# Kernel tuning notes

Measured on AMD Instinct MI355X. Metric: run time of the kernel, lower is better.

The kernel has to match this reference:

```python
import jax, jax.numpy as jnp
import numpy as np


def setup_inputs() -> dict:
    key = jax.random.key(0)
    k1, k2, k3 = jax.random.split(key, 3)
    B, N, D = 4096, 8192, 1024
    protein_features = jax.random.normal(k1, (B, D), dtype=jnp.float32)
    function_features = jax.random.normal(k2, (N, D), dtype=jnp.float32)
    positive_mask = jax.random.randint(k3, (B, N), 0, 2, dtype=jnp.int32)
    temperature = jnp.zeros((1,), dtype=jnp.float32)  # exp(0) = 1
    return {
        "protein_features": protein_features,
        "function_features": function_features,
        "positive_mask": positive_mask,
        "temperature": temperature,
    }


def reference(protein_features, function_features, positive_mask, temperature):
    # logits: [B, N]
    logits = jnp.matmul(protein_features, function_features.T) / jnp.exp(temperature[0])
    # row-wise logsumexp, computed ONCE per row (the torch loop recomputes it per positive)
    lse = jax.nn.logsumexp(logits, axis=1, keepdims=True)  # [B, 1]
    m = (positive_mask == 1).astype(logits.dtype)          # [B, N]
    n_pos = m.sum()
    # per-pair loss = -pos_logit + logsumexp(row); mean over all positive pairs
    loss_sum = ((lse - logits) * m).sum()
    return jnp.where(n_pos > 0, loss_sum / n_pos, jnp.zeros((), dtype=logits.dtype))
```

## Files before the change

kernel.cpp:

```cpp
#include <hip/hip_runtime.h>
#include <hip/hip_bf16.h>

typedef __attribute__((ext_vector_type(4))) float f32x4;
typedef __attribute__((ext_vector_type(8))) __bf16 bf16x8;
typedef __attribute__((ext_vector_type(8))) unsigned short u16x8;

constexpr int BROWS = 4096;
constexpr int NCOLS = 8192;
constexpr int DK    = 1024;
constexpr int BM = 128, BN = 128, BK = 64;
constexpr int NCB = NCOLS / BN;
constexpr int NKT = DK / BK;
constexpr int NIT = NKT / 2;

__device__ static inline unsigned short f2bf(float f) {
  unsigned int u = __builtin_bit_cast(unsigned int, f);
  u += 0x7FFFu + ((u >> 16) & 1u);
  return (unsigned short)(u >> 16);
}

__device__ static inline void gload16(const void* g, void* l) {
  __builtin_amdgcn_global_load_lds(
      (const __attribute__((address_space(1))) void*)g,
      (__attribute__((address_space(3))) void*)l, 16, 0, 0);
}

__global__ void convert_kernel(const float* __restrict__ src,
                               unsigned short* __restrict__ dst,
                               int n4, int applyScale,
                               const float* __restrict__ temp) {
  float scale = applyScale ? expf(-temp[0]) : 1.0f;
  int i = blockIdx.x * blockDim.x + threadIdx.x;
  if (i >= n4) return;
  float4 v = reinterpret_cast<const float4*>(src)[i];
  ushort4 o;
  o.x = f2bf(v.x * scale);
  o.y = f2bf(v.y * scale);
  o.z = f2bf(v.z * scale);
  o.w = f2bf(v.w * scale);
  reinterpret_cast<ushort4*>(dst)[i] = o;
}

__device__ __forceinline__ void stage_tile(const unsigned short* __restrict__ g,
                                           unsigned short* l, int t, int kt) {
#pragma unroll
  for (int p = 0; p < 4; ++p) {
    const int off = p * 4096 + t * 16;
    const int row = off >> 7;
    const int keSw = ((off & 127) >> 1) ^ ((row & 7) << 3);
    gload16(g + (size_t)row * DK + kt * 64 + keSw, l + (off >> 1));
  }
}

#define MFMA_BF16 __builtin_amdgcn_mfma_f32_16x16x32_bf16

#define LDS_FRAG(base, row, kk)                                             \
  __builtin_bit_cast(bf16x8, *reinterpret_cast<const u16x8*>(               \
      &(base)[((row) * 64 + (kk) * 32 + l4 * 8) ^ (((row) & 7) << 3)]))

#define READ_A(buf, q)                                                  \
  aFr[0][0] = LDS_FRAG(buf, wm * 64 + (2*(q)    )*16 + l15, 0);         \
  aFr[0][1] = LDS_FRAG(buf, wm * 64 + (2*(q)    )*16 + l15, 1);         \
  aFr[1][0] = LDS_FRAG(buf, wm * 64 + (2*(q) + 1)*16 + l15, 0);         \
  aFr[1][1] = LDS_FRAG(buf, wm * 64 + (2*(q) + 1)*16 + l15, 1);

#define READ_B(buf)                                                     \
  bFr[0][0] = LDS_FRAG(buf, wn * 64 +  0 + l15, 0);                     \
  bFr[0][1] = LDS_FRAG(buf, wn * 64 +  0 + l15, 1);                     \
  bFr[1][0] = LDS_FRAG(buf, wn * 64 + 16 + l15, 0);                     \
  bFr[1][1] = LDS_FRAG(buf, wn * 64 + 16 + l15, 1);                     \
  bFr[2][0] = LDS_FRAG(buf, wn * 64 + 32 + l15, 0);                     \
  bFr[2][1] = LDS_FRAG(buf, wn * 64 + 32 + l15, 1);                     \
  bFr[3][0] = LDS_FRAG(buf, wn * 64 + 48 + l15, 0);                     \
  bFr[3][1] = LDS_FRAG(buf, wn * 64 + 48 + l15, 1);

#define COMPUTE(q)                                                                  \
  __builtin_amdgcn_s_setprio(1);                                                   \
  _Pragma("unroll") for (int mm = 0; mm < 2; ++mm)                                  \
  _Pragma("unroll") for (int n = 0; n < 4; ++n) {                                   \
    acc[2*(q)+mm][n] = MFMA_BF16(aFr[mm][0], bFr[n][0], acc[2*(q)+mm][n], 0, 0, 0); \
    acc[2*(q)+mm][n] = MFMA_BF16(aFr[mm][1], bFr[n][1], acc[2*(q)+mm][n], 0, 0, 0); \
  }                                                                                 \
  __builtin_amdgcn_s_setprio(0);

#define PHASE_MID                                    \
  __builtin_amdgcn_s_barrier();                      \
  asm volatile("s_waitcnt lgkmcnt(0)" ::: "memory");

#define PHASE_END                                    \
  __builtin_amdgcn_s_barrier();

__global__ __launch_bounds__(256, 2)
void main_kernel(const unsigned short* __restrict__ Pb,
                 const unsigned short* __restrict__ Fb,
                 const int* __restrict__ mask,
                 f32x4* __restrict__ partials) {
  __shared__ __align__(16) unsigned short Ab[2][128 * 64];
  __shared__ __align__(16) unsigned short Bb[2][128 * 64];
  __shared__ float redM[2][128], redS[2][128], redP[2][128], redC[2][128];

  const int t    = threadIdx.x;
  const int lane = t & 63;
  const int w    = t >> 6;
  const int wm   = w >> 1;
  const int wn   = w & 1;
  const int l15  = lane & 15;
  const int l4   = lane >> 4;

  const int brow = blockIdx.y * BM;
  const int bcol = blockIdx.x * BN;

  const unsigned short* Ag = Pb + (size_t)brow * DK;
  const unsigned short* Bg = Fb + (size_t)bcol * DK;

  f32x4 acc[4][4] = {};
  bf16x8 bFr[4][2];
  bf16x8 aFr[2][2];

  stage_tile(Ag, Ab[0], t, 0);
  stage_tile(Bg, Bb[0], t, 0);
  asm volatile("s_waitcnt vmcnt(0)" ::: "memory");
  __builtin_amdgcn_s_barrier();

  for (int j = 0; j < NIT; ++j) {
    const int t0 = 2 * j, t1 = 2 * j + 1;
    const bool more = (j < NIT - 1);
    READ_B(Bb[0]); READ_A(Ab[0], 0);
    stage_tile(Ag, Ab[1], t, t1);
    asm volatile("s_waitcnt vmcnt(4)" ::: "memory");
    PHASE_MID; COMPUTE(0); PHASE_END;
    READ_A(Ab[0], 1);
    stage_tile(Bg, Bb[1], t, t1);
    PHASE_MID; COMPUTE(1); PHASE_END;
    READ_B(Bb[1]); READ_A(Ab[1], 0);
    if (more) {
      stage_tile(Ag, Ab[0], t, t0 + 2);
      asm volatile("s_waitcnt vmcnt(4)" ::: "memory");
    } else {
      asm volatile("s_waitcnt vmcnt(0)" ::: "memory");
    }
    PHASE_MID; COMPUTE(0); PHASE_END;
    READ_A(Ab[1], 1);
    if (more) stage_tile(Bg, Bb[0], t, t0 + 2);
    PHASE_MID; COMPUTE(1); PHASE_END;
  }

#pragma unroll
  for (int m = 0; m < 4; ++m) {
#pragma unroll
    for (int r = 0; r < 4; ++r) {
      float v0 = acc[m][0][r], v1 = acc[m][1][r], v2 = acc[m][2][r], v3 = acc[m][3][r];
      float mx = fmaxf(fmaxf(v0, v1), fmaxf(v2, v3));
#pragma unroll
      for (int s = 1; s < 16; s <<= 1) mx = fmaxf(mx, __shfl_xor(mx, s, 64));
      float se = __expf(v0 - mx) + __expf(v1 - mx) + __expf(v2 - mx) + __expf(v3 - mx);

      const int lr = wm * 64 + m * 16 + l4 * 4 + r;
      const int* mrow = mask + (size_t)(brow + lr) * NCOLS + bcol + wn * 64 + l15;
      float ps = 0.f, pc = 0.f;
      if (mrow[0]  == 1) { ps += v0; pc += 1.f; }
      if (mrow[16] == 1) { ps += v1; pc += 1.f; }
      if (mrow[32] == 1) { ps += v2; pc += 1.f; }
      if (mrow[48] == 1) { ps += v3; pc += 1.f; }
#pragma unroll
      for (int s = 1; s < 16; s <<= 1) {
        se += __shfl_xor(se, s, 64);
        ps += __shfl_xor(ps, s, 64);
        pc += __shfl_xor(pc, s, 64);
      }
      if (l15 == 0) {
        redM[wn][lr] = mx;
        redS[wn][lr] = se;
        redP[wn][lr] = ps;
        redC[wn][lr] = pc;
      }
    }
  }
  __syncthreads();

  if (t < 128) {
    float m0 = redM[0][t], m1 = redM[1][t];
    float m  = fmaxf(m0, m1);
    float s  = redS[0][t] * __expf(m0 - m) + redS[1][t] * __expf(m1 - m);
    float ps = redP[0][t] + redP[1][t];
    float pc = redC[0][t] + redC[1][t];
    f32x4 out4;
    out4.x = m; out4.y = s; out4.z = ps; out4.w = pc;
    partials[(size_t)(brow + t) * NCB + blockIdx.x] = out4;
  }
}

__global__ void row_reduce_kernel(const f32x4* __restrict__ partials,
                                  float* __restrict__ rowContrib,
                                  float* __restrict__ rowCnt) {
  const int row  = blockIdx.x * 4 + (threadIdx.x >> 6);
  const int lane = threadIdx.x & 63;
  f32x4 p = partials[(size_t)row * NCB + lane];
  float m = p.x;
#pragma unroll
  for (int s = 1; s < 64; s <<= 1) m = fmaxf(m, __shfl_xor(m, s, 64));
  float se = p.y * __expf(p.x - m);
  float ps = p.z, pc = p.w;
#pragma unroll
  for (int s = 1; s < 64; s <<= 1) {
    se += __shfl_xor(se, s, 64);
    ps += __shfl_xor(ps, s, 64);
    pc += __shfl_xor(pc, s, 64);
  }
  if (lane == 0) {
    float lse = m + logf(se);
    rowContrib[row] = pc * lse - ps;
    rowCnt[row]     = pc;
  }
}

__global__ void final_kernel(const float* __restrict__ rowContrib,
                             const float* __restrict__ rowCnt,
                             float* __restrict__ out) {
  __shared__ double sC[256];
  __shared__ double sN[256];
  double c = 0.0, n = 0.0;
  for (int i = threadIdx.x; i < BROWS; i += 256) {
    c += (double)rowContrib[i];
    n += (double)rowCnt[i];
  }
  sC[threadIdx.x] = c;
  sN[threadIdx.x] = n;
  __syncthreads();
  for (int s = 128; s > 0; s >>= 1) {
    if ((int)threadIdx.x < s) {
      sC[threadIdx.x] += sC[threadIdx.x + s];
      sN[threadIdx.x] += sN[threadIdx.x + s];
    }
    __syncthreads();
  }
  if (threadIdx.x == 0) out[0] = (sN[0] > 0.0) ? (float)(sC[0] / sN[0]) : 0.0f;
}

extern "C" void kernel_launch(void* const* d_in, const int* in_sizes, int n_in,
                              void* d_out, int out_size, void* d_ws, size_t ws_size,
                              hipStream_t stream) {
  const float* P    = (const float*)d_in[0];
  const float* F    = (const float*)d_in[1];
  const int*   mask = (const int*)d_in[2];
  const float* temp = (const float*)d_in[3];
  float* out = (float*)d_out;

  char* ws = (char*)d_ws;
  unsigned short* Pb = (unsigned short*)ws;
  unsigned short* Fb = (unsigned short*)(ws + (size_t)BROWS * DK * 2);
  f32x4* partials    = (f32x4*)(ws + (size_t)(BROWS + NCOLS) * DK * 2);
  float* rowContrib  = (float*)((char*)partials + (size_t)BROWS * NCB * sizeof(f32x4));
  float* rowCnt      = rowContrib + BROWS;

  const int nP4 = BROWS * DK / 4;
  const int nF4 = NCOLS * DK / 4;
  hipLaunchKernelGGL(convert_kernel, dim3(nP4 / 256), dim3(256), 0, stream, P, Pb, nP4, 1, temp);
  hipLaunchKernelGGL(convert_kernel, dim3(nF4 / 256), dim3(256), 0, stream, F, Fb, nF4, 0, temp);
  hipLaunchKernelGGL(main_kernel, dim3(NCOLS / BN, BROWS / BM), dim3(256), 0, stream, Pb, Fb, mask, partials);
  hipLaunchKernelGGL(row_reduce_kernel, dim3(BROWS / 4), dim3(256), 0, stream, partials, rowContrib, rowCnt);
  hipLaunchKernelGGL(final_kernel, dim3(1), dim3(256), 0, stream, rowContrib, rowCnt, out);
}
```

Before: 129.2 us.

## Replace double-buffered phased GEMM loop with single-buffer loop at higher occupancy

Removes the double-buffered LDS ping-pong schedule with split phases and barriers. In its place is a simple single-buffer loop that stages each K tile, syncs, then reads fragments and runs the MFMAs. LDS use is halved and launch bounds are raised to 4 blocks per CU, so latency is hidden by more resident waves instead of explicit prefetch. The cost is that global loads no longer overlap compute within a block, and register pressure is tighter under the higher occupancy bound.

```diff
diff --git a/kernel.cpp b/kernel.cpp
--- a/kernel.cpp
+++ b/kernel.cpp
@@ -11,7 +11,6 @@
 constexpr int BM = 128, BN = 128, BK = 64;
 constexpr int NCB = NCOLS / BN;
 constexpr int NKT = DK / BK;
-constexpr int NIT = NKT / 2;
 
 __device__ static inline unsigned short f2bf(float f) {
   unsigned int u = __builtin_bit_cast(unsigned int, f);
@@ -58,45 +57,13 @@
   __builtin_bit_cast(bf16x8, *reinterpret_cast<const u16x8*>(               \
       &(base)[((row) * 64 + (kk) * 32 + l4 * 8) ^ (((row) & 7) << 3)]))
 
-#define READ_A(buf, q)                                                  \
-  aFr[0][0] = LDS_FRAG(buf, wm * 64 + (2*(q)    )*16 + l15, 0);         \
-  aFr[0][1] = LDS_FRAG(buf, wm * 64 + (2*(q)    )*16 + l15, 1);         \
-  aFr[1][0] = LDS_FRAG(buf, wm * 64 + (2*(q) + 1)*16 + l15, 0);         \
-  aFr[1][1] = LDS_FRAG(buf, wm * 64 + (2*(q) + 1)*16 + l15, 1);
-
-#define READ_B(buf)                                                     \
-  bFr[0][0] = LDS_FRAG(buf, wn * 64 +  0 + l15, 0);                     \
-  bFr[0][1] = LDS_FRAG(buf, wn * 64 +  0 + l15, 1);                     \
-  bFr[1][0] = LDS_FRAG(buf, wn * 64 + 16 + l15, 0);                     \
-  bFr[1][1] = LDS_FRAG(buf, wn * 64 + 16 + l15, 1);                     \
-  bFr[2][0] = LDS_FRAG(buf, wn * 64 + 32 + l15, 0);                     \
-  bFr[2][1] = LDS_FRAG(buf, wn * 64 + 32 + l15, 1);                     \
-  bFr[3][0] = LDS_FRAG(buf, wn * 64 + 48 + l15, 0);                     \
-  bFr[3][1] = LDS_FRAG(buf, wn * 64 + 48 + l15, 1);
-
-#define COMPUTE(q)                                                                  \
-  __builtin_amdgcn_s_setprio(1);                                                   \
-  _Pragma("unroll") for (int mm = 0; mm < 2; ++mm)                                  \
-  _Pragma("unroll") for (int n = 0; n < 4; ++n) {                                   \
-    acc[2*(q)+mm][n] = MFMA_BF16(aFr[mm][0], bFr[n][0], acc[2*(q)+mm][n], 0, 0, 0); \
-    acc[2*(q)+mm][n] = MFMA_BF16(aFr[mm][1], bFr[n][1], acc[2*(q)+mm][n], 0, 0, 0); \
-  }                                                                                 \
-  __builtin_amdgcn_s_setprio(0);
-
-#define PHASE_MID                                    \
-  __builtin_amdgcn_s_barrier();                      \
-  asm volatile("s_waitcnt lgkmcnt(0)" ::: "memory");
-
-#define PHASE_END                                    \
-  __builtin_amdgcn_s_barrier();
-
-__global__ __launch_bounds__(256, 2)
+__global__ __launch_bounds__(256, 4)
 void main_kernel(const unsigned short* __restrict__ Pb,
                  const unsigned short* __restrict__ Fb,
                  const int* __restrict__ mask,
                  f32x4* __restrict__ partials) {
-  __shared__ __align__(16) unsigned short Ab[2][128 * 64];
-  __shared__ __align__(16) unsigned short Bb[2][128 * 64];
+  __shared__ __align__(16) unsigned short Ab[128 * 64];
+  __shared__ __align__(16) unsigned short Bb[128 * 64];
   __shared__ float redM[2][128], redS[2][128], redP[2][128], redC[2][128];
 
   const int t    = threadIdx.x;
@@ -114,35 +81,33 @@
   const unsigned short* Bg = Fb + (size_t)bcol * DK;
 
   f32x4 acc[4][4] = {};
-  bf16x8 bFr[4][2];
-  bf16x8 aFr[2][2];
-
-  stage_tile(Ag, Ab[0], t, 0);
-  stage_tile(Bg, Bb[0], t, 0);
-  asm volatile("s_waitcnt vmcnt(0)" ::: "memory");
-  __builtin_amdgcn_s_barrier();
-
-  for (int j = 0; j < NIT; ++j) {
-    const int t0 = 2 * j, t1 = 2 * j + 1;
-    const bool more = (j < NIT - 1);
-    READ_B(Bb[0]); READ_A(Ab[0], 0);
-    stage_tile(Ag, Ab[1], t, t1);
-    asm volatile("s_waitcnt vmcnt(4)" ::: "memory");
-    PHASE_MID; COMPUTE(0); PHASE_END;
-    READ_A(Ab[0], 1);
-    stage_tile(Bg, Bb[1], t, t1);
-    PHASE_MID; COMPUTE(1); PHASE_END;
-    READ_B(Bb[1]); READ_A(Ab[1], 0);
-    if (more) {
-      stage_tile(Ag, Ab[0], t, t0 + 2);
-      asm volatile("s_waitcnt vmcnt(4)" ::: "memory");
-    } else {
-      asm volatile("s_waitcnt vmcnt(0)" ::: "memory");
-    }
-    PHASE_MID; COMPUTE(0); PHASE_END;
-    READ_A(Ab[1], 1);
-    if (more) stage_tile(Bg, Bb[0], t, t0 + 2);
-    PHASE_MID; COMPUTE(1); PHASE_END;
+
+  for (int kt = 0; kt < NKT; ++kt) {
+    if (kt) __syncthreads();
+    stage_tile(Ag, Ab, t, kt);
+    stage_tile(Bg, Bb, t, kt);
+    __syncthreads();
+
+    bf16x8 aFr[4][2], bFr[4][2];
+#pragma unroll
+    for (int m = 0; m < 4; ++m) {
+      aFr[m][0] = LDS_FRAG(Ab, wm * 64 + m * 16 + l15, 0);
+      aFr[m][1] = LDS_FRAG(Ab, wm * 64 + m * 16 + l15, 1);
+    }
+#pragma unroll
+    for (int n = 0; n < 4; ++n) {
+      bFr[n][0] = LDS_FRAG(Bb, wn * 64 + n * 16 + l15, 0);
+      bFr[n][1] = LDS_FRAG(Bb, wn * 64 + n * 16 + l15, 1);
+    }
+    __builtin_amdgcn_s_setprio(1);
+#pragma unroll
+    for (int m = 0; m < 4; ++m)
+#pragma unroll
+      for (int n = 0; n < 4; ++n) {
+        acc[m][n] = MFMA_BF16(aFr[m][0], bFr[n][0], acc[m][n], 0, 0, 0);
+        acc[m][n] = MFMA_BF16(aFr[m][1], bFr[n][1], acc[m][n], 0, 0, 0);
+      }
+    __builtin_amdgcn_s_setprio(0);
   }
 
 #pragma unroll
```

Result: slower. 343.4 us (+165.9%).
